# Kernel optimization log

Measured on AMD Instinct MI355X. Metric: run time of the kernel, lower is better.

Reference implementation:

```python
import jax, jax.numpy as jnp
import numpy as np
from jax import lax

EPS = 1e-8
DN = ('NCHW', 'OIHW', 'NCHW')


def setup_inputs() -> dict:
    key = jax.random.key(0)
    k1, k2 = jax.random.split(key)
    inputs = jax.random.normal(k1, (16, 3, 512, 512), dtype=jnp.float32)
    template = jax.random.normal(k2, (16, 3, 21, 21), dtype=jnp.float32)
    return {"inputs": inputs, "template": template}


def _normalize_template(template):
    # Z-normalize each (batch, channel) plane independently, then divide by
    # patch element count (matches NCC.__init__).
    B, C, th, tw = template.shape
    t = template.reshape(B, C, th * tw)
    t = t - jnp.mean(t, axis=-1, keepdims=True)
    t = t / (jnp.std(t, axis=-1, keepdims=True) + EPS)  # ddof=0 == unbiased=False
    return t.reshape(B, C, th, tw) / (th * tw)


def reference(inputs, template):
    B, C, H, W = inputs.shape
    th, tw = template.shape[2], template.shape[3]
    nt = _normalize_template(template)

    # Per-(b,c) depthwise cross-correlation (the grouped conv with eye-masked
    # weights is exactly a depthwise conv with per-sample filters).
    x = inputs.reshape(1, B * C, H, W)
    w = nt.reshape(B * C, 1, th, tw)
    res = lax.conv_general_dilated(x, w, (1, 1), 'VALID',
                                   dimension_numbers=DN,
                                   feature_group_count=B * C)
    res = res.reshape(B, C, res.shape[2], res.shape[3])  # (B,C,Hout,Wout)

    # Local (patch) std per channel via box filter (shared across batch).
    box = jnp.full((C, 1, th, tw), 1.0 / (th * tw), dtype=inputs.dtype)
    mean = lax.conv_general_dilated(inputs, box, (1, 1), 'VALID',
                                    dimension_numbers=DN, feature_group_count=C)
    mean_sq = lax.conv_general_dilated(inputs * inputs, box, (1, 1), 'VALID',
                                       dimension_numbers=DN, feature_group_count=C)
    std = jnp.sqrt(mean_sq - mean * mean + EPS)

    return res / (std + EPS)
```

## Files before the change

### kernel.cpp

```cpp
#include <hip/hip_runtime.h>
#include <math.h>

typedef __attribute__((ext_vector_type(8)))  short short8;
typedef __attribute__((ext_vector_type(16))) float f32x16;

#define NPLANE 48
#define H 512
#define W 512
#define TH 21
#define OH 492
#define OW 492
#define EPSF 1e-8f

#define STRIDE 168
#define SEG_ROWS 84

#define BONES_HOFF (4128768u / 2)

__device__ inline unsigned short f2bf(float f) {
    unsigned u = __float_as_uint(f);
    return (unsigned short)((u + 0x7FFFu + ((u >> 16) & 1u)) >> 16);
}
__device__ inline float bf2f(unsigned s) {
    return __uint_as_float(s << 16);
}

__global__ void build_b_kernel(const float* __restrict__ tpl,
                               unsigned short* __restrict__ ws16) {
    __shared__ float sm[2];
    const int plane = blockIdx.x;
    const float* t = tpl + plane * 441;
    const int tid = threadIdx.x;
    if (tid < 64) {
        float s = 0.f, s2 = 0.f;
        for (int k = tid; k < 441; k += 64) {
            float x = t[k];
            s += x; s2 += x * x;
        }
#pragma unroll
        for (int o = 32; o >= 1; o >>= 1) {
            s  += __shfl_down(s, o);
            s2 += __shfl_down(s2, o);
        }
        if (tid == 0) {
            float mean = s / 441.f;
            float var = fmaxf(s2 / 441.f - mean * mean, 0.f);
            sm[0] = mean;
            sm[1] = 1.f / ((sqrtf(var) + EPSF) * 441.f);
        }
    }
    __syncthreads();
    const float mean = sm[0], scale = sm[1];

    unsigned short* bc = ws16 + (size_t)plane * 43008;
    for (int i = tid; i < 43008; i += 256) {
        int j = i & 7, lane = (i >> 3) & 63, s = (i >> 9) & 3, u = i >> 11;
        int k = ((lane >> 5) << 3) + j, n = lane & 31;
        int v = 16 * s + k - n;
        float val = (v >= 0 && v < TH) ? (t[u * 21 + v] - mean) * scale : 0.f;
        bc[i] = f2bf(val);
    }
    if (plane == 0) {
        unsigned short* bo = ws16 + BONES_HOFF;
        const unsigned short one = f2bf(1.f);
        for (int i = tid; i < 2048; i += 256) {
            int j = i & 7, lane = (i >> 3) & 63, s = (i >> 9) & 3;
            int k = ((lane >> 5) << 3) + j, n = lane & 31;
            int v = 16 * s + k - n;
            bo[i] = (v >= 0 && v < TH) ? one : (unsigned short)0;
        }
    }
}

__global__ __launch_bounds__(256, 3) void ncc_fused_kernel(
    const float* __restrict__ in, const unsigned short* __restrict__ ws16,
    float* __restrict__ out) {
    __shared__ short seg[SEG_ROWS * STRIDE];
    __shared__ short vbuf[64 * STRIDE];

    const int plane = blockIdx.z;
    const int x0 = blockIdx.x * 128;
    const int y0 = blockIdx.y * 64;
    const int tid = threadIdx.x;
    const int lane = tid & 63;
    const int tr = (tid >> 6) & 1;
    const int tc = tid >> 7;
    const float* src = in + (size_t)plane * H * W;

    for (int i = tid; i < SEG_ROWS * 20; i += 256) {
        int row = i / 20, s8 = i - row * 20;
        int gy = y0 + row, gx = x0 + s8 * 8;
        short8 val;
        if (gy < H && gx + 7 < W) {
            float4 a = *(const float4*)(src + gy * W + gx);
            float4 b = *(const float4*)(src + gy * W + gx + 4);
            val[0] = (short)f2bf(a.x); val[1] = (short)f2bf(a.y);
            val[2] = (short)f2bf(a.z); val[3] = (short)f2bf(a.w);
            val[4] = (short)f2bf(b.x); val[5] = (short)f2bf(b.y);
            val[6] = (short)f2bf(b.z); val[7] = (short)f2bf(b.w);
        } else {
#pragma unroll
            for (int e = 0; e < 8; ++e) {
                float xv = (gy < H && gx + e < W) ? src[gy * W + gx + e] : 0.f;
                val[e] = (short)f2bf(xv);
            }
        }
        *(short8*)&seg[row * STRIDE + s8 * 8] = val;
    }
    __syncthreads();

    const int m = lane & 31;
    const int half = lane >> 5;
    const int abase = (tr * 32 + m) * STRIDE + tc * 64 + half * 8;
    const unsigned short* bc = ws16 + (size_t)plane * 43008 + lane * 8;

    f32x16 acc[2];
#pragma unroll
    for (int t = 0; t < 2; ++t)
#pragma unroll
        for (int e = 0; e < 16; ++e) acc[t][e] = 0.f;

    short8 bf[4], bfn[4];
#pragma unroll
    for (int s = 0; s < 4; ++s)
        bf[s] = *(const short8*)(bc + s * 512);

    for (int u = 0; u < TH; ++u) {
        const int un = (u + 1 < TH) ? u + 1 : 0;
#pragma unroll
        for (int s = 0; s < 4; ++s)
            bfn[s] = *(const short8*)(bc + (un * 4 + s) * 512);

        short8 af[6];
#pragma unroll
        for (int g = 0; g < 6; ++g)
            af[g] = *(const short8*)&seg[abase + u * STRIDE + g * 16];

#pragma unroll
        for (int t = 0; t < 2; ++t) {
#pragma unroll
            for (int s = 0; s < 4; ++s)
                acc[t] = __builtin_amdgcn_mfma_f32_32x32x16_bf16(
                    af[2 * t + s], bf[s], acc[t], 0, 0, 0);
        }
#pragma unroll
        for (int s = 0; s < 4; ++s) bf[s] = bfn[s];
    }

    const unsigned short* bo16 = ws16 + BONES_HOFF + lane * 8;
    short8 bones[4];
#pragma unroll
    for (int s = 0; s < 4; ++s)
        bones[s] = *(const short8*)(bo16 + s * 512);

    if (tid < 160) {
        const int hr = (tid >= 80) ? 32 : 0;
        const int c2 = (tid % 80) * 2;
        float s0 = 0.f, s1 = 0.f;
#pragma unroll
        for (int r = 0; r < 20; ++r) {
            unsigned p = *(const unsigned*)&seg[(hr + r) * STRIDE + c2];
            s0 += bf2f(p & 0xffffu);
            s1 += bf2f(p >> 16);
        }
        for (int y = hr; y < hr + 32; ++y) {
            unsigned p = *(const unsigned*)&seg[(y + 20) * STRIDE + c2];
            s0 += bf2f(p & 0xffffu);
            s1 += bf2f(p >> 16);
            *(unsigned*)&vbuf[y * STRIDE + c2] =
                (unsigned)f2bf(s0) | ((unsigned)f2bf(s1) << 16);
            unsigned q = *(const unsigned*)&seg[y * STRIDE + c2];
            s0 -= bf2f(q & 0xffffu);
            s1 -= bf2f(q >> 16);
        }
    }
    __syncthreads();

    f32x16 aS[2];
#pragma unroll
    for (int t = 0; t < 2; ++t) {
#pragma unroll
        for (int e = 0; e < 16; ++e) aS[t][e] = 0.f;
#pragma unroll
        for (int s = 0; s < 4; ++s) {
            short8 vf = *(const short8*)&vbuf[abase + (2 * t + s) * 16];
            aS[t] = __builtin_amdgcn_mfma_f32_32x32x16_bf16(vf, bones[s],
                                                            aS[t], 0, 0, 0);
        }
    }
    __syncthreads();

    if (tid < 160) {
        const int hr = (tid >= 80) ? 32 : 0;
        const int c2 = (tid % 80) * 2;
        float s0 = 0.f, s1 = 0.f;
#pragma unroll
        for (int r = 0; r < 20; ++r) {
            unsigned p = *(const unsigned*)&seg[(hr + r) * STRIDE + c2];
            float a = bf2f(p & 0xffffu), b = bf2f(p >> 16);
            s0 = fmaf(a, a, s0);
            s1 = fmaf(b, b, s1);
        }
        for (int y = hr; y < hr + 32; ++y) {
            unsigned p = *(const unsigned*)&seg[(y + 20) * STRIDE + c2];
            float a = bf2f(p & 0xffffu), b = bf2f(p >> 16);
            s0 = fmaf(a, a, s0);
            s1 = fmaf(b, b, s1);
            *(unsigned*)&vbuf[y * STRIDE + c2] =
                (unsigned)f2bf(s0) | ((unsigned)f2bf(s1) << 16);
            unsigned q = *(const unsigned*)&seg[y * STRIDE + c2];
            float c = bf2f(q & 0xffffu), d = bf2f(q >> 16);
            s0 = fmaf(-c, c, s0);
            s1 = fmaf(-d, d, s1);
        }
    }
    __syncthreads();

    const float invn = 1.f / 441.f;
    float* outp = out + (size_t)plane * OH * OW;
#pragma unroll
    for (int t = 0; t < 2; ++t) {
        f32x16 aQ;
#pragma unroll
        for (int e = 0; e < 16; ++e) aQ[e] = 0.f;
#pragma unroll
        for (int s = 0; s < 4; ++s) {
            short8 qf = *(const short8*)&vbuf[abase + (2 * t + s) * 16];
            aQ = __builtin_amdgcn_mfma_f32_32x32x16_bf16(qf, bones[s], aQ,
                                                         0, 0, 0);
        }
        const int gx = x0 + tc * 64 + t * 32 + (lane & 31);
        if (gx < OW) {
#pragma unroll
            for (int r = 0; r < 16; ++r) {
                int gy = y0 + tr * 32 + (r & 3) + ((r >> 2) << 3) + half * 4;
                if (gy < OH) {
                    float mean = aS[t][r] * invn;
                    float msq = aQ[r] * invn;
                    float sd = sqrtf(msq - mean * mean + EPSF);
                    outp[(size_t)gy * OW + gx] = acc[t][r] / (sd + EPSF);
                }
            }
        }
    }
}

extern "C" void kernel_launch(void* const* d_in, const int* in_sizes, int n_in,
                              void* d_out, int out_size, void* d_ws,
                              size_t ws_size, hipStream_t stream) {
    const float* inputs = (const float*)d_in[0];
    const float* tmpl = (const float*)d_in[1];
    float* out = (float*)d_out;
    unsigned short* ws16 = (unsigned short*)d_ws;

    build_b_kernel<<<NPLANE, 256, 0, stream>>>(tmpl, ws16);
    ncc_fused_kernel<<<dim3(4, 8, NPLANE), 256, 0, stream>>>(inputs, ws16, out);
}
```

Baseline: 164.0 us.

## Halve box-filter LDS buffer, raise occupancy to 4 blocks, use packed bf16 convert

```diff
diff --git a/kernel.cpp b/kernel.cpp
--- a/kernel.cpp
+++ b/kernel.cpp
@@ -23,6 +23,11 @@
 }
 __device__ inline float bf2f(unsigned s) {
     return __uint_as_float(s << 16);
+}
+__device__ inline unsigned cvtpk(float lo, float hi) {
+    unsigned r;
+    asm("v_cvt_pk_bf16_f32 %0, %1, %2" : "=v"(r) : "v"(lo), "v"(hi));
+    return r;
 }
 
 __global__ void build_b_kernel(const float* __restrict__ tpl,
@@ -72,11 +77,11 @@
     }
 }
 
-__global__ __launch_bounds__(256, 3) void ncc_fused_kernel(
+__global__ __launch_bounds__(256, 4) void ncc_fused_kernel(
     const float* __restrict__ in, const unsigned short* __restrict__ ws16,
     float* __restrict__ out) {
     __shared__ short seg[SEG_ROWS * STRIDE];
-    __shared__ short vbuf[64 * STRIDE];
+    __shared__ short vbuf[32 * STRIDE];
 
     const int plane = blockIdx.z;
     const int x0 = blockIdx.x * 128;
@@ -90,28 +95,31 @@
     for (int i = tid; i < SEG_ROWS * 20; i += 256) {
         int row = i / 20, s8 = i - row * 20;
         int gy = y0 + row, gx = x0 + s8 * 8;
-        short8 val;
         if (gy < H && gx + 7 < W) {
             float4 a = *(const float4*)(src + gy * W + gx);
             float4 b = *(const float4*)(src + gy * W + gx + 4);
-            val[0] = (short)f2bf(a.x); val[1] = (short)f2bf(a.y);
-            val[2] = (short)f2bf(a.z); val[3] = (short)f2bf(a.w);
-            val[4] = (short)f2bf(b.x); val[5] = (short)f2bf(b.y);
-            val[6] = (short)f2bf(b.z); val[7] = (short)f2bf(b.w);
+            uint4 v;
+            v.x = cvtpk(a.x, a.y);
+            v.y = cvtpk(a.z, a.w);
+            v.z = cvtpk(b.x, b.y);
+            v.w = cvtpk(b.z, b.w);
+            *(uint4*)&seg[row * STRIDE + s8 * 8] = v;
         } else {
+            short8 val;
 #pragma unroll
             for (int e = 0; e < 8; ++e) {
                 float xv = (gy < H && gx + e < W) ? src[gy * W + gx + e] : 0.f;
                 val[e] = (short)f2bf(xv);
             }
-        }
-        *(short8*)&seg[row * STRIDE + s8 * 8] = val;
+            *(short8*)&seg[row * STRIDE + s8 * 8] = val;
+        }
     }
     __syncthreads();
 
     const int m = lane & 31;
     const int half = lane >> 5;
     const int abase = (tr * 32 + m) * STRIDE + tc * 64 + half * 8;
+    const int vbase = m * STRIDE + tc * 64 + half * 8;
     const unsigned short* bc = ws16 + (size_t)plane * 43008 + lane * 8;
 
     f32x16 acc[2];
@@ -120,129 +128,143 @@
 #pragma unroll
         for (int e = 0; e < 16; ++e) acc[t][e] = 0.f;
 
-    short8 bf[4], bfn[4];
-#pragma unroll
-    for (int s = 0; s < 4; ++s)
-        bf[s] = *(const short8*)(bc + s * 512);
-
-    for (int u = 0; u < TH; ++u) {
-        const int un = (u + 1 < TH) ? u + 1 : 0;
-#pragma unroll
-        for (int s = 0; s < 4; ++s)
-            bfn[s] = *(const short8*)(bc + (un * 4 + s) * 512);
-
+    auto corr_step = [&](int u, short8* bf) {
         short8 af[6];
 #pragma unroll
         for (int g = 0; g < 6; ++g)
             af[g] = *(const short8*)&seg[abase + u * STRIDE + g * 16];
-
-#pragma unroll
-        for (int t = 0; t < 2; ++t) {
+#pragma unroll
+        for (int t = 0; t < 2; ++t)
 #pragma unroll
             for (int s = 0; s < 4; ++s)
                 acc[t] = __builtin_amdgcn_mfma_f32_32x32x16_bf16(
                     af[2 * t + s], bf[s], acc[t], 0, 0, 0);
-        }
-#pragma unroll
-        for (int s = 0; s < 4; ++s) bf[s] = bfn[s];
-    }
-
-    const unsigned short* bo16 = ws16 + BONES_HOFF + lane * 8;
-    short8 bones[4];
+    };
+
+    short8 bA[4], bB[4];
 #pragma unroll
     for (int s = 0; s < 4; ++s)
-        bones[s] = *(const short8*)(bo16 + s * 512);
-
-    if (tid < 160) {
-        const int hr = (tid >= 80) ? 32 : 0;
-        const int c2 = (tid % 80) * 2;
-        float s0 = 0.f, s1 = 0.f;
-#pragma unroll
-        for (int r = 0; r < 20; ++r) {
-            unsigned p = *(const unsigned*)&seg[(hr + r) * STRIDE + c2];
-            s0 += bf2f(p & 0xffffu);
-            s1 += bf2f(p >> 16);
-        }
-        for (int y = hr; y < hr + 32; ++y) {
-            unsigned p = *(const unsigned*)&seg[(y + 20) * STRIDE + c2];
-            s0 += bf2f(p & 0xffffu);
-            s1 += bf2f(p >> 16);
-            *(unsigned*)&vbuf[y * STRIDE + c2] =
-                (unsigned)f2bf(s0) | ((unsigned)f2bf(s1) << 16);
-            unsigned q = *(const unsigned*)&seg[y * STRIDE + c2];
-            s0 -= bf2f(q & 0xffffu);
-            s1 -= bf2f(q >> 16);
-        }
-    }
-    __syncthreads();
+        bA[s] = *(const short8*)(bc + s * 512);
+
+    for (int u = 0; u < TH - 1; u += 2) {
+#pragma unroll
+        for (int s = 0; s < 4; ++s)
+            bB[s] = *(const short8*)(bc + ((u + 1) * 4 + s) * 512);
+        corr_step(u, bA);
+#pragma unroll
+        for (int s = 0; s < 4; ++s)
+            bA[s] = *(const short8*)(bc + ((u + 2) * 4 + s) * 512);
+        corr_step(u + 1, bB);
+    }
+    corr_step(TH - 1, bA);
+
+    auto vpass = [&](int Hh, bool sq) {
+        if (tid < 160) {
+            const int sub = (tid >= 80) ? 16 : 0;
+            const int c2 = (tid % 80) * 2;
+            const int base = Hh * 32 + sub;
+            float s0 = 0.f, s1 = 0.f;
+#pragma unroll
+            for (int r = 0; r < 20; ++r) {
+                unsigned p = *(const unsigned*)&seg[(base + r) * STRIDE + c2];
+                float a = bf2f(p & 0xffffu), b = bf2f(p >> 16);
+                if (sq) { s0 = fmaf(a, a, s0); s1 = fmaf(b, b, s1); }
+                else    { s0 += a; s1 += b; }
+            }
+            for (int yb = 0; yb < 16; yb += 8) {
+                unsigned pin[8], pout[8];
+#pragma unroll
+                for (int r = 0; r < 8; ++r) {
+                    pin[r]  = *(const unsigned*)
+                        &seg[(base + yb + r + 20) * STRIDE + c2];
+                    pout[r] = *(const unsigned*)
+                        &seg[(base + yb + r) * STRIDE + c2];
+                }
+#pragma unroll
+                for (int r = 0; r < 8; ++r) {
+                    float a = bf2f(pin[r] & 0xffffu), b = bf2f(pin[r] >> 16);
+                    if (sq) { s0 = fmaf(a, a, s0); s1 = fmaf(b, b, s1); }
+                    else    { s0 += a; s1 += b; }
+                    *(unsigned*)&vbuf[(sub + yb + r) * STRIDE + c2] =
+                        cvtpk(s0, s1);
+                    float c = bf2f(pout[r] & 0xffffu), d = bf2f(pout[r] >> 16);
+                    if (sq) { s0 = fmaf(-c, c, s0); s1 = fmaf(-d, d, s1); }
+                    else    { s0 -= c; s1 -= d; }
+                }
+            }
+        }
+    };
 
     f32x16 aS[2];
-#pragma unroll
-    for (int t = 0; t < 2; ++t) {
-#pragma unroll
-        for (int e = 0; e < 16; ++e) aS[t][e] = 0.f;
-#pragma unroll
-        for (int s = 0; s < 4; ++s) {
-            short8 vf = *(const short8*)&vbuf[abase + (2 * t + s) * 16];
-            aS[t] = __builtin_amdgcn_mfma_f32_32x32x16_bf16(vf, bones[s],
-                                                            aS[t], 0, 0, 0);
-        }
-    }
-    __syncthreads();
-
-    if (tid < 160) {
-        const int hr = (tid >= 80) ? 32 : 0;
-        const int c2 = (tid % 80) * 2;
-        float s0 = 0.f, s1 = 0.f;
-#pragma unroll
-        for (int r = 0; r < 20; ++r) {
-            unsigned p = *(const unsigned*)&seg[(hr + r) * STRIDE + c2];
-            float a = bf2f(p & 0xffffu), b = bf2f(p >> 16);
-            s0 = fmaf(a, a, s0);
-            s1 = fmaf(b, b, s1);
-        }
-        for (int y = hr; y < hr + 32; ++y) {
-            unsigned p = *(const unsigned*)&seg[(y + 20) * STRIDE + c2];
-            float a = bf2f(p & 0xffffu), b = bf2f(p >> 16);
-            s0 = fmaf(a, a, s0);
-            s1 = fmaf(b, b, s1);
-            *(unsigned*)&vbuf[y * STRIDE + c2] =
-                (unsigned)f2bf(s0) | ((unsigned)f2bf(s1) << 16);
-            unsigned q = *(const unsigned*)&seg[y * STRIDE + c2];
-            float c = bf2f(q & 0xffffu), d = bf2f(q >> 16);
-            s0 = fmaf(-c, c, s0);
-            s1 = fmaf(-d, d, s1);
-        }
-    }
-    __syncthreads();
-
-    const float invn = 1.f / 441.f;
-    float* outp = out + (size_t)plane * OH * OW;
-#pragma unroll
-    for (int t = 0; t < 2; ++t) {
-        f32x16 aQ;
-#pragma unroll
-        for (int e = 0; e < 16; ++e) aQ[e] = 0.f;
-#pragma unroll
-        for (int s = 0; s < 4; ++s) {
-            short8 qf = *(const short8*)&vbuf[abase + (2 * t + s) * 16];
-            aQ = __builtin_amdgcn_mfma_f32_32x32x16_bf16(qf, bones[s], aQ,
-                                                         0, 0, 0);
-        }
-        const int gx = x0 + tc * 64 + t * 32 + (lane & 31);
-        if (gx < OW) {
-#pragma unroll
-            for (int r = 0; r < 16; ++r) {
-                int gy = y0 + tr * 32 + (r & 3) + ((r >> 2) << 3) + half * 4;
-                if (gy < OH) {
-                    float mean = aS[t][r] * invn;
-                    float msq = aQ[r] * invn;
-                    float sd = sqrtf(msq - mean * mean + EPSF);
-                    outp[(size_t)gy * OW + gx] = acc[t][r] / (sd + EPSF);
+    auto box = [&](f32x16* dst) {
+        const unsigned short* bo16 = ws16 + BONES_HOFF + lane * 8;
+        short8 bn[4];
+#pragma unroll
+        for (int s = 0; s < 4; ++s)
+            bn[s] = *(const short8*)(bo16 + s * 512);
+#pragma unroll
+        for (int t = 0; t < 2; ++t) {
+#pragma unroll
+            for (int e = 0; e < 16; ++e) dst[t][e] = 0.f;
+#pragma unroll
+            for (int s = 0; s < 4; ++s) {
+                short8 vf = *(const short8*)&vbuf[vbase + (2 * t + s) * 16];
+                dst[t] = __builtin_amdgcn_mfma_f32_32x32x16_bf16(
+                    vf, bn[s], dst[t], 0, 0, 0);
+            }
+        }
+    };
+
+    auto finish = [&]() {
+        const unsigned short* bo16 = ws16 + BONES_HOFF + lane * 8;
+        short8 bn[4];
+#pragma unroll
+        for (int s = 0; s < 4; ++s)
+            bn[s] = *(const short8*)(bo16 + s * 512);
+        const float invn = 1.f / 441.f;
+        float* outp = out + (size_t)plane * OH * OW;
+#pragma unroll
+        for (int t = 0; t < 2; ++t) {
+            f32x16 q;
+#pragma unroll
+            for (int e = 0; e < 16; ++e) q[e] = 0.f;
+#pragma unroll
+            for (int s = 0; s < 4; ++s) {
+                short8 qf = *(const short8*)&vbuf[vbase + (2 * t + s) * 16];
+                q = __builtin_amdgcn_mfma_f32_32x32x16_bf16(qf, bn[s], q,
+                                                            0, 0, 0);
+            }
+            const int gx = x0 + tc * 64 + t * 32 + m;
+            if (gx < OW) {
+#pragma unroll
+                for (int r = 0; r < 16; ++r) {
+                    int gy = y0 + tr * 32 + (r & 3) + ((r >> 2) << 3) + half * 4;
+                    if (gy < OH) {
+                        float mean = aS[t][r] * invn;
+                        float msq = q[r] * invn;
+                        float sd = sqrtf(msq - mean * mean + EPSF);
+                        outp[(size_t)gy * OW + gx] = acc[t][r] / (sd + EPSF);
+                    }
                 }
             }
         }
-    }
+    };
+
+    vpass(0, false);
+    __syncthreads();
+    if (tr == 0) box(aS);
+    __syncthreads();
+    vpass(1, false);
+    __syncthreads();
+    if (tr == 1) box(aS);
+    __syncthreads();
+    vpass(0, true);
+    __syncthreads();
+    if (tr == 0) finish();
+    __syncthreads();
+    vpass(1, true);
+    __syncthreads();
+    if (tr == 1) finish();
 }
 
 extern "C" void kernel_launch(void* const* d_in, const int* in_sizes, int n_in,
```

Result: no change. 165.8 us (+1.1%).
